# Optimization experiments

Measured on AMD Instinct MI355X. Metric: run time of the kernel, lower is better.

The kernel has to match this reference:

```python
import jax, jax.numpy as jnp
import numpy as np

H = 128; TIME_DIM = 8; LAM = 0.01; NUM_LAYERS = 2; B = 64
N_FACT = 100000; N_COMP = 5000; E = 500000; D_FACT = 384; D_COMP = 64
MLP_IN = 2 + 2 * (TIME_DIM // 2) + 1  # 11


def setup_inputs() -> dict:
    key = jax.random.key(0)
    ks = jax.random.split(key, 40)
    rn = lambda k, sh, s=0.05: jax.random.normal(k, sh, jnp.float32) * s
    inp = {
        'x_fact': jax.random.normal(ks[0], (N_FACT, D_FACT), jnp.float32),
        'x_comp': jax.random.normal(ks[1], (N_COMP, D_COMP), jnp.float32),
        'ea_f2c': jax.random.uniform(ks[2], (E, 2), jnp.float32),
        'ea_c2f': jax.random.uniform(ks[3], (E, 2), jnp.float32),
        'ei_f2c_src': jax.random.randint(ks[4], (E,), 0, N_FACT, jnp.int32),
        'ei_f2c_dst': jax.random.randint(ks[5], (E,), 0, N_COMP, jnp.int32),
        'ei_c2f_src': jax.random.randint(ks[6], (E,), 0, N_COMP, jnp.int32),
        'ei_c2f_dst': jax.random.randint(ks[7], (E,), 0, N_FACT, jnp.int32),
        'fact_batch': jnp.sort(jax.random.randint(ks[8], (N_FACT,), 0, B, jnp.int32)),
        'comp_batch': jnp.sort(jax.random.randint(ks[9], (N_COMP,), 0, B, jnp.int32)),
        # lazy per-type input projections
        'W_in_fact': rn(ks[10], (D_FACT, H)), 'b_in_fact': jnp.zeros((H,), jnp.float32),
        'W_in_comp': rn(ks[11], (D_COMP, H)), 'b_in_comp': jnp.zeros((H,), jnp.float32),
        # EdgeAttrEncoder MLP: 11 -> 32 -> 16 -> 1
        'eW1': rn(ks[12], (MLP_IN, 32)), 'eb1': jnp.zeros((32,), jnp.float32),
        'eW2': rn(ks[13], (32, 16)), 'eb2': jnp.zeros((16,), jnp.float32),
        'eW3': rn(ks[14], (16, 1)), 'eb3': jnp.zeros((1,), jnp.float32),
        # GraphConv per layer (axis0) per edge type (axis1: 0=f->c, 1=c->f)
        'W_rel': rn(ks[15], (NUM_LAYERS, 2, H, H)), 'b_rel': jnp.zeros((NUM_LAYERS, 2, H), jnp.float32),
        'W_root': rn(ks[16], (NUM_LAYERS, 2, H, H)),
        # shared post LayerNorm per node type (axis0: 0=fact, 1=company)
        'ln_scale': jnp.ones((2, H), jnp.float32), 'ln_bias': jnp.zeros((2, H), jnp.float32),
        # classifier 2H -> H -> 1
        'Wc1': rn(ks[17], (2 * H, H)), 'bc1': jnp.zeros((H,), jnp.float32),
        'Wc2': rn(ks[18], (H, 1)), 'bc2': jnp.zeros((1,), jnp.float32),
    }
    return inp


def _edge_gate(ea, eW1, eb1, eW2, eb2, eW3, eb3):
    # ea: [E,2] -> gate [E]
    sent = jnp.clip(ea[:, 0:1], -1.0, 1.0)
    decay = ea[:, 1:2]
    # decay in [0,1] -> delta_t = -log(decay)/lambda, clamped >= 0
    dt = jnp.maximum(-jnp.log(jnp.clip(decay, 1e-6, None)) / LAM, 0.0)
    ds = jnp.clip(dt / 30.0, 0.0, 12.0)
    freqs = jnp.arange(1, TIME_DIM // 2 + 1, dtype=ds.dtype)
    tvec = jnp.concatenate([jnp.sin(ds * freqs), jnp.cos(ds * freqs), ds], axis=-1)
    x = jnp.concatenate([sent, jnp.log1p(dt), tvec], axis=-1)  # [E,11]
    h = jax.nn.relu(x @ eW1 + eb1)
    h = jax.nn.relu(h @ eW2 + eb2)
    return jax.nn.sigmoid(h @ eW3 + eb3)[:, 0]


def _layernorm(x, scale, bias, eps=1e-5):
    mu = jnp.mean(x, axis=-1, keepdims=True)
    var = jnp.var(x, axis=-1, keepdims=True)
    return (x - mu) * jax.lax.rsqrt(var + eps) * scale + bias


def _seg_mean(x, seg, n):
    s = jax.ops.segment_sum(x, seg, num_segments=n)
    c = jax.ops.segment_sum(jnp.ones((x.shape[0], 1), x.dtype), seg, num_segments=n)
    return s / jnp.maximum(c, 1.0)


def reference(x_fact, x_comp, ea_f2c, ea_c2f, ei_f2c_src, ei_f2c_dst, ei_c2f_src,
              ei_c2f_dst, fact_batch, comp_batch, W_in_fact, b_in_fact, W_in_comp,
              b_in_comp, eW1, eb1, eW2, eb2, eW3, eb3, W_rel, b_rel, W_root,
              ln_scale, ln_bias, Wc1, bc1, Wc2, bc2):
    # per-type input projection + ReLU
    xf = jax.nn.relu(x_fact @ W_in_fact + b_in_fact)   # [N_fact, H]
    xc = jax.nn.relu(x_comp @ W_in_comp + b_in_comp)   # [N_comp, H]
    # MLP-gated edge weights (shared encoder across relations)
    w_f2c = _edge_gate(ea_f2c, eW1, eb1, eW2, eb2, eW3, eb3)  # [E]
    w_c2f = _edge_gate(ea_c2f, eW1, eb1, eW2, eb2, eW3, eb3)  # [E]
    nf, nc = xf.shape[0], xc.shape[0]
    for l in range(NUM_LAYERS):
        prev_f, prev_c = xf, xc
        # GraphConv: lin_rel(sum_j w_ij * x_j) + lin_root(x_i)  (aggr='add')
        agg_c = jax.ops.segment_sum(xf[ei_f2c_src] * w_f2c[:, None], ei_f2c_dst, num_segments=nc)
        new_c = agg_c @ W_rel[l, 0] + b_rel[l, 0] + xc @ W_root[l, 0]
        agg_f = jax.ops.segment_sum(xc[ei_c2f_src] * w_c2f[:, None], ei_c2f_dst, num_segments=nf)
        new_f = agg_f @ W_rel[l, 1] + b_rel[l, 1] + xf @ W_root[l, 1]
        # ReLU -> residual -> shared per-type LayerNorm
        xf = _layernorm(jax.nn.relu(new_f) + prev_f, ln_scale[0], ln_bias[0])
        xc = _layernorm(jax.nn.relu(new_c) + prev_c, ln_scale[1], ln_bias[1])
    fact_pool = _seg_mean(xf, fact_batch, B)   # [B, H]
    comp_pool = _seg_mean(xc, comp_batch, B)   # [B, H]
    pooled = jnp.concatenate([fact_pool, comp_pool], axis=-1)  # [B, 2H]
    h = jax.nn.relu(pooled @ Wc1 + bc1)
    return (h @ Wc2 + bc2)[:, 0]  # [B] logits
```

## Files before the change

### kernel.cpp

```cpp
#include <hip/hip_runtime.h>
#include <math.h>

#define H 128
#define EDGES 500000
#define NFACT 100000
#define NCOMP 5000
#define BATCH 64

typedef _Float16 half8_t __attribute__((ext_vector_type(8)));
typedef float floatx4 __attribute__((ext_vector_type(4)));

__device__ inline short4 f4_to_h4(float4 v){
  union { short4 s; _Float16 h[4]; } u;
  u.h[0]=(_Float16)v.x; u.h[1]=(_Float16)v.y; u.h[2]=(_Float16)v.z; u.h[3]=(_Float16)v.w;
  return u.s;
}

__device__ inline half8_t f8_to_h8(float4 a, float4 b){
  half8_t r;
  r[0]=(_Float16)a.x; r[1]=(_Float16)a.y; r[2]=(_Float16)a.z; r[3]=(_Float16)a.w;
  r[4]=(_Float16)b.x; r[5]=(_Float16)b.y; r[6]=(_Float16)b.z; r[7]=(_Float16)b.w;
  return r;
}

__global__ void k_hist(const int* __restrict__ dst, int n, int* __restrict__ cnt){
  for (int e = blockIdx.x*blockDim.x + threadIdx.x; e < n; e += gridDim.x*blockDim.x)
    atomicAdd(&cnt[dst[e]], 1);
}

__global__ __launch_bounds__(1024) void k_scan1(const int* __restrict__ cnt, int n,
                                                int* __restrict__ offs, int* __restrict__ part){
  __shared__ int sh[1024];
  int tid = threadIdx.x;
  int i = blockIdx.x*1024 + tid;
  int v = (i < n) ? cnt[i] : 0;
  sh[tid] = v;
  __syncthreads();
  for (int d = 1; d < 1024; d <<= 1){
    int t = (tid >= d) ? sh[tid-d] : 0;
    __syncthreads();
    sh[tid] += t;
    __syncthreads();
  }
  if (i < n) offs[i] = sh[tid] - v;
  if (tid == 1023) part[blockIdx.x] = sh[1023];
}

__global__ void k_scan2(int* part, int nb){
  __shared__ int sh[128];
  int tid = threadIdx.x;
  int v = (tid < nb) ? part[tid] : 0;
  sh[tid] = v;
  __syncthreads();
  for (int d = 1; d < 128; d <<= 1){
    int t = (tid >= d) ? sh[tid-d] : 0;
    __syncthreads();
    sh[tid] += t;
    __syncthreads();
  }
  if (tid < nb) part[tid] = sh[tid] - v;
}

__global__ __launch_bounds__(1024) void k_scan3(int* offs, int n, const int* __restrict__ part, int total){
  int i = blockIdx.x*1024 + threadIdx.x;
  if (i < n) offs[i] += part[blockIdx.x];
  if (i == 0) offs[n] = total;
}

__global__ void k_fill2(const int* __restrict__ src, const int* __restrict__ dst,
                        const float* __restrict__ w, int n, const int* __restrict__ offs,
                        int* __restrict__ cur, int4* __restrict__ ed){
  for (int e = blockIdx.x*blockDim.x + threadIdx.x; e < n; e += gridDim.x*blockDim.x){
    int d = dst[e];
    int p = offs[d] + atomicAdd(&cur[d], 1);
    ed[p] = make_int4(src[e], __float_as_int(w[e]), d, 0);
  }
}

__global__ __launch_bounds__(256) void k_prep(const float* __restrict__ W_in,
                                              const float* __restrict__ W_rel,
                                              const float* __restrict__ W_root,
                                              _Float16* __restrict__ wt_in,
                                              _Float16* __restrict__ wcat0,
                                              _Float16* __restrict__ wcat1){
  int i = blockIdx.x*256 + threadIdx.x;
  if (i < 49152){
    int n = i / 384, k = i % 384;
    wt_in[i] = (_Float16)W_in[k*128 + n];
  } else if (i < 49152 + 32768){
    int j = i - 49152;
    int n = j / 256, k = j % 256;
    const float* Wr = W_rel  + 1*16384;
    const float* Wo = W_root + 1*16384;
    wcat0[j] = (_Float16)(k < 128 ? Wr[k*128+n] : Wo[(k-128)*128+n]);
  } else if (i < 49152 + 65536){
    int j = i - 49152 - 32768;
    int n = j / 256, k = j % 256;
    const float* Wr = W_rel  + 3*16384;
    const float* Wo = W_root + 3*16384;
    wcat1[j] = (_Float16)(k < 128 ? Wr[k*128+n] : Wo[(k-128)*128+n]);
  }
}

__global__ __launch_bounds__(256) void k_gate(const float* __restrict__ ea,
                       const float* __restrict__ eW1, const float* __restrict__ eb1,
                       const float* __restrict__ eW2, const float* __restrict__ eb2,
                       const float* __restrict__ eW3, const float* __restrict__ eb3,
                       float* __restrict__ wout, int n){
  __shared__ float w1[11*32], b1[32], w2[32*16], b2[16], w3[16];
  __shared__ float b3;
  int tid = threadIdx.x;
  for (int i = tid; i < 11*32; i += blockDim.x) w1[i] = eW1[i];
  for (int i = tid; i < 32;    i += blockDim.x) b1[i] = eb1[i];
  for (int i = tid; i < 32*16; i += blockDim.x) w2[i] = eW2[i];
  for (int i = tid; i < 16;    i += blockDim.x) b2[i] = eb2[i];
  for (int i = tid; i < 16;    i += blockDim.x) w3[i] = eW3[i];
  if (tid == 0) b3 = eb3[0];
  __syncthreads();
  for (int e = blockIdx.x*blockDim.x + tid; e < n; e += gridDim.x*blockDim.x){
    float2 eav = ((const float2*)ea)[e];
    float sent  = fminf(fmaxf(eav.x, -1.f), 1.f);
    float decay = eav.y;
    float dt = fmaxf(-logf(fmaxf(decay, 1e-6f)) * 100.f, 0.f);
    float ds = fminf(dt * (1.f/30.f), 12.f);
    float s1 = sinf(ds), c1 = cosf(ds);
    float s2v = 2.f*s1*c1;
    float c2v = 1.f - 2.f*s1*s1;
    float s3v = s1*c2v + c1*s2v;
    float c3v = c1*c2v - s1*s2v;
    float s4v = 2.f*s2v*c2v;
    float c4v = 1.f - 2.f*s2v*s2v;
    float x[11];
    x[0] = sent; x[1] = log1pf(dt);
    x[2] = s1;  x[3] = s2v; x[4] = s3v; x[5] = s4v;
    x[6] = c1;  x[7] = c2v; x[8] = c3v; x[9] = c4v;
    x[10] = ds;
    float s2[16];
    #pragma unroll
    for (int j = 0; j < 16; j++) s2[j] = b2[j];
    #pragma unroll
    for (int i = 0; i < 32; i++){
      float h = b1[i];
      #pragma unroll
      for (int k = 0; k < 11; k++) h += x[k]*w1[k*32+i];
      h = fmaxf(h, 0.f);
      #pragma unroll
      for (int j = 0; j < 16; j++) s2[j] += h*w2[i*16+j];
    }
    float o = b3;
    #pragma unroll
    for (int j = 0; j < 16; j++) o += fmaxf(s2[j], 0.f)*w3[j];
    wout[e] = 1.f/(1.f + expf(-o));
  }
}

template<int K, int R>
__global__ __launch_bounds__(128) void k_input_s(const float* __restrict__ X, const float* __restrict__ W,
                                                 const float* __restrict__ bias, float* __restrict__ Y){
  __shared__ float xs[R*K];
  int t = threadIdx.x;
  long row0 = (long)blockIdx.x * R;
  const float4* src = (const float4*)(X + row0*K);
  float4* d4 = (float4*)xs;
  for (int i = t; i < R*K/4; i += 128) d4[i] = src[i];
  __syncthreads();
  float acc[R];
  #pragma unroll
  for (int r = 0; r < R; r++) acc[r] = 0.f;
  for (int k4 = 0; k4 < K/4; k4++){
    int kb = k4*4;
    float w0 = W[(kb+0)*H+t], w1 = W[(kb+1)*H+t], w2 = W[(kb+2)*H+t], w3 = W[(kb+3)*H+t];
    #pragma unroll
    for (int r = 0; r < R; r++){
      float4 xv = ((const float4*)(xs + r*K))[k4];
      acc[r] += xv.x*w0 + xv.y*w1 + xv.z*w2 + xv.w*w3;
    }
  }
  float b = bias[t];
  #pragma unroll
  for (int r = 0; r < R; r++)
    Y[(row0+r)*H + t] = fmaxf(acc[r] + b, 0.f);
}

__global__ __launch_bounds__(256, 3) void k_input_m(const float* __restrict__ X,
                                                 const _Float16* __restrict__ Wt,
                                                 const float* __restrict__ bias,
                                                 float* __restrict__ Y){
  int lane = threadIdx.x & 63;
  int wv = threadIdx.x >> 6;
  long row0 = ((long)blockIdx.x*4 + wv) * 16;
  if (row0 >= NFACT) return;
  int m = lane & 15, q = lane >> 4;
  const float4* xrow = (const float4*)(X + (row0 + m)*384 + q*8);
  const _Float16* wb0 = Wt + (size_t)m*384 + q*8;
  float4 xa[12], xb[12];
  #pragma unroll
  for (int ks = 0; ks < 12; ks++){
    xa[ks] = xrow[ks*8];
    xb[ks] = xrow[ks*8 + 1];
  }
  floatx4 acc[8];
  #pragma unroll
  for (int nt = 0; nt < 8; nt++) acc[nt] = (floatx4){0.f,0.f,0.f,0.f};
  #pragma unroll
  for (int ks = 0; ks < 12; ks++){
    half8_t av = f8_to_h8(xa[ks], xb[ks]);
    #pragma unroll
    for (int nt = 0; nt < 8; nt++){
      half8_t bv = *(const half8_t*)(wb0 + (size_t)nt*16*384 + ks*32);
      acc[nt] = __builtin_amdgcn_mfma_f32_16x16x32_f16(av, bv, acc[nt], 0, 0, 0);
    }
  }
  #pragma unroll
  for (int nt = 0; nt < 8; nt++){
    int col = nt*16 + m;
    float b = bias[col];
    #pragma unroll
    for (int i = 0; i < 4; i++)
      Y[(row0 + q*4 + i)*H + col] = fmaxf(acc[nt][i] + b, 0.f);
  }
}

__global__ __launch_bounds__(64) void k_layer_m(
    const float* __restrict__ xsrc, const float* __restrict__ xprev,
    const int* __restrict__ offs, const int4* __restrict__ ed,
    const _Float16* __restrict__ Wt, const float* __restrict__ brel,
    const float* __restrict__ lnsc, const float* __restrict__ lnbi,
    float* __restrict__ xnext){
  __shared__ _Float16 xin[16][264];
  int t = threadIdx.x, c = t & 31, g = t >> 5;
  long row0 = (long)blockIdx.x * 16;
  int grow0 = g*8;
  #pragma unroll
  for (int j = 0; j < 8; j++){
    int lr = grow0 + j;
    ((short4*)&xin[lr][0])[c] = make_short4(0,0,0,0);
    float4 pv = ((const float4*)(xprev + (row0+lr)*H))[c];
    ((short4*)&xin[lr][128])[c] = f4_to_h4(pv);
  }
  int lo = offs[row0 + grow0], hi = offs[row0 + grow0 + 8];
  float4 a = make_float4(0.f,0.f,0.f,0.f);
  int cur = (int)row0 + grow0;
  int idx = lo;
  for (; idx + 8 <= hi; idx += 8){
    int4 mrec[8];
    #pragma unroll
    for (int j = 0; j < 8; j++) mrec[j] = ed[idx+j];
    float4 v[8];
    #pragma unroll
    for (int j = 0; j < 8; j++) v[j] = ((const float4*)(xsrc + (long)mrec[j].x*H))[c];
    #pragma unroll
    for (int j = 0; j < 8; j++){
      float w = __int_as_float(mrec[j].y);
      if (mrec[j].z != cur){ ((short4*)&xin[cur-(int)row0][0])[c] = f4_to_h4(a); a = make_float4(0.f,0.f,0.f,0.f); cur = mrec[j].z; }
      a.x += v[j].x*w; a.y += v[j].y*w; a.z += v[j].z*w; a.w += v[j].w*w;
    }
  }
  for (; idx < hi; idx++){
    int4 mrec = ed[idx];
    float4 v = ((const float4*)(xsrc + (long)mrec.x*H))[c];
    float w = __int_as_float(mrec.y);
    if (mrec.z != cur){ ((short4*)&xin[cur-(int)row0][0])[c] = f4_to_h4(a); a = make_float4(0.f,0.f,0.f,0.f); cur = mrec.z; }
    a.x += v.x*w; a.y += v.y*w; a.z += v.z*w; a.w += v.w*w;
  }
  if (lo < hi) ((short4*)&xin[cur-(int)row0][0])[c] = f4_to_h4(a);

  int m = t & 15, q = t >> 4;
  floatx4 acc[8];
  #pragma unroll
  for (int nt = 0; nt < 8; nt++) acc[nt] = (floatx4){0.f,0.f,0.f,0.f};
  #pragma unroll
  for (int ks = 0; ks < 8; ks++){
    half8_t av = *(const half8_t*)&xin[m][ks*32 + q*8];
    #pragma unroll
    for (int nt = 0; nt < 8; nt++){
      half8_t bv = *(const half8_t*)(Wt + (size_t)(nt*16 + m)*256 + ks*32 + q*8);
      acc[nt] = __builtin_amdgcn_mfma_f32_16x16x32_f16(av, bv, acc[nt], 0, 0, 0);
    }
  }
  float vs[8][4];
  float s[4] = {0.f,0.f,0.f,0.f}, ss[4] = {0.f,0.f,0.f,0.f};
  #pragma unroll
  for (int nt = 0; nt < 8; nt++){
    int col = nt*16 + m;
    float b = brel[col];
    #pragma unroll
    for (int i = 0; i < 4; i++){
      int lr = q*4 + i;
      float pv = (float)xin[lr][128 + col];
      float v = fmaxf(acc[nt][i] + b, 0.f) + pv;
      vs[nt][i] = v;
      s[i] += v; ss[i] += v*v;
    }
  }
  #pragma unroll
  for (int i = 0; i < 4; i++){
    #pragma unroll
    for (int mm = 1; mm < 16; mm <<= 1){
      s[i]  += __shfl_xor(s[i],  mm, 64);
      ss[i] += __shfl_xor(ss[i], mm, 64);
    }
  }
  #pragma unroll
  for (int nt = 0; nt < 8; nt++){
    int col = nt*16 + m;
    float lsc = lnsc[col], lbi = lnbi[col];
    #pragma unroll
    for (int i = 0; i < 4; i++){
      float mu  = s[i]*(1.f/H);
      float var = ss[i]*(1.f/H) - mu*mu;
      float rstd = rsqrtf(var + 1e-5f);
      xnext[(row0 + q*4 + i)*H + col] = (vs[nt][i] - mu)*rstd*lsc + lbi;
    }
  }
}

template<int R>
__global__ __launch_bounds__(128) void k_layer(
    const float* __restrict__ xsrc, const float* __restrict__ xprev,
    const int* __restrict__ offs, const int4* __restrict__ ed,
    const float* __restrict__ Wrel, const float* __restrict__ brel,
    const float* __restrict__ Wroot, const float* __restrict__ lnsc,
    const float* __restrict__ lnbi, float* __restrict__ xnext){
  constexpr int RG = R/4;
  __shared__ float xin[R][256];
  int t = threadIdx.x, c = t & 31, g = t >> 5;
  long row0 = (long)blockIdx.x * R;
  int grow0 = g*RG;
  #pragma unroll
  for (int j = 0; j < RG; j++){
    int lr = grow0 + j;
    ((float4*)&xin[lr][0])[c] = make_float4(0.f,0.f,0.f,0.f);
    ((float4*)&xin[lr][128])[c] = ((const float4*)(xprev + (row0+lr)*H))[c];
  }
  int lo = offs[row0 + grow0], hi = offs[row0 + grow0 + RG];
  float4 a = make_float4(0.f,0.f,0.f,0.f);
  int cur = (int)row0 + grow0;
  int idx = lo;
  for (; idx + 8 <= hi; idx += 8){
    int4 m[8];
    #pragma unroll
    for (int j = 0; j < 8; j++) m[j] = ed[idx+j];
    float4 v[8];
    #pragma unroll
    for (int j = 0; j < 8; j++) v[j] = ((const float4*)(xsrc + (long)m[j].x*H))[c];
    #pragma unroll
    for (int j = 0; j < 8; j++){
      float w = __int_as_float(m[j].y);
      if (m[j].z != cur){ ((float4*)&xin[cur-(int)row0][0])[c] = a; a = make_float4(0.f,0.f,0.f,0.f); cur = m[j].z; }
      a.x += v[j].x*w; a.y += v[j].y*w; a.z += v[j].z*w; a.w += v[j].w*w;
    }
  }
  for (; idx < hi; idx++){
    int4 m = ed[idx];
    float4 v = ((const float4*)(xsrc + (long)m.x*H))[c];
    float w = __int_as_float(m.y);
    if (m.z != cur){ ((float4*)&xin[cur-(int)row0][0])[c] = a; a = make_float4(0.f,0.f,0.f,0.f); cur = m.z; }
    a.x += v.x*w; a.y += v.y*w; a.z += v.z*w; a.w += v.w*w;
  }
  if (lo < hi) ((float4*)&xin[cur-(int)row0][0])[c] = a;

  float4 acc[RG];
  float4 bv = ((const float4*)brel)[c];
  #pragma unroll
  for (int j = 0; j < RG; j++) acc[j] = bv;
  #pragma unroll
  for (int p = 0; p < 2; p++){
    const float4* Wp = (const float4*)(p ? Wroot : Wrel) + c;
    #pragma unroll 4
    for (int k4 = 0; k4 < 32; k4++){
      float4 xv[RG];
      #pragma unroll
      for (int j = 0; j < RG; j++)
        xv[j] = ((const float4*)xin[grow0+j])[p*32 + k4];
      #pragma unroll
      for (int kk = 0; kk < 4; kk++){
        float4 wv = Wp[(size_t)(k4*4+kk)*32];
        #pragma unroll
        for (int j = 0; j < RG; j++){
          float xk = (kk==0) ? xv[j].x : (kk==1) ? xv[j].y : (kk==2) ? xv[j].z : xv[j].w;
          acc[j].x += xk*wv.x; acc[j].y += xk*wv.y; acc[j].z += xk*wv.z; acc[j].w += xk*wv.w;
        }
      }
    }
  }
  float4 lsc = ((const float4*)lnsc)[c];
  float4 lbi = ((const float4*)lnbi)[c];
  #pragma unroll
  for (int j = 0; j < RG; j++){
    int lr = grow0 + j;
    float4 pv = ((const float4*)&xin[lr][128])[c];
    float4 v;
    v.x = fmaxf(acc[j].x, 0.f) + pv.x;
    v.y = fmaxf(acc[j].y, 0.f) + pv.y;
    v.z = fmaxf(acc[j].z, 0.f) + pv.z;
    v.w = fmaxf(acc[j].w, 0.f) + pv.w;
    float s  = v.x + v.y + v.z + v.w;
    float ss = v.x*v.x + v.y*v.y + v.z*v.z + v.w*v.w;
    #pragma unroll
    for (int mm = 1; mm < 32; mm <<= 1){ s += __shfl_xor(s, mm, 64); ss += __shfl_xor(ss, mm, 64); }
    float mu  = s*(1.f/H);
    float var = ss*(1.f/H) - mu*mu;
    float rstd = rsqrtf(var + 1e-5f);
    float4 o;
    o.x = (v.x - mu)*rstd*lsc.x + lbi.x;
    o.y = (v.y - mu)*rstd*lsc.y + lbi.y;
    o.z = (v.z - mu)*rstd*lsc.z + lbi.z;
    o.w = (v.w - mu)*rstd*lsc.w + lbi.w;
    ((float4*)(xnext + (row0+lr)*H))[c] = o;
  }
}

#define PCHUNK 128
#define FBLK ((NFACT + PCHUNK - 1) / PCHUNK)
#define CBLK ((NCOMP + PCHUNK - 1) / PCHUNK)

__global__ __launch_bounds__(128) void k_pool_acc(const float* __restrict__ xf, const float* __restrict__ xc,
                                                  const int* __restrict__ fb, const int* __restrict__ cb,
                                                  float* __restrict__ pooled){
  int t = threadIdx.x;
  int b = blockIdx.x;
  if (b < FBLK){
    int start = b*PCHUNK, end = start + PCHUNK; if (end > NFACT) end = NFACT;
    float s = 0.f; int curb = -1;
    for (int i = start; i < end; i++){
      int bb = fb[i];
      if (bb != curb){
        if (curb >= 0) atomicAdd(&pooled[curb*256 + t], s);
        curb = bb; s = 0.f;
      }
      s += xf[(long)i*H + t];
    }
    if (curb >= 0) atomicAdd(&pooled[curb*256 + t], s);
  } else {
    int bbk = b - FBLK;
    int start = bbk*PCHUNK, end = start + PCHUNK; if (end > NCOMP) end = NCOMP;
    float s = 0.f; int curb = -1;
    for (int i = start; i < end; i++){
      int bb = cb[i];
      if (bb != curb){
        if (curb >= 0) atomicAdd(&pooled[curb*256 + 128 + t], s);
        curb = bb; s = 0.f;
      }
      s += xc[(long)i*H + t];
    }
    if (curb >= 0) atomicAdd(&pooled[curb*256 + 128 + t], s);
  }
}

__device__ inline int lowerb(const int* a, int n, int key){
  int lo = 0, hi = n;
  while (lo < hi){ int m = (lo+hi) >> 1; if (a[m] < key) lo = m+1; else hi = m; }
  return lo;
}

__global__ __launch_bounds__(128) void k_head(const float* __restrict__ pooled,
                                              const int* __restrict__ fb, const int* __restrict__ cb,
                                              const float* __restrict__ Wc1, const float* __restrict__ bc1,
                                              const float* __restrict__ Wc2, const float* __restrict__ bc2,
                                              float* __restrict__ out){
  __shared__ float p[256];
  __shared__ float red[2];
  int t = threadIdx.x, b = blockIdx.x;
  int flo = lowerb(fb, NFACT, b), fhi = lowerb(fb, NFACT, b+1);
  int clo = lowerb(cb, NCOMP, b), chi = lowerb(cb, NCOMP, b+1);
  float fc = (float)((fhi - flo) > 1 ? (fhi - flo) : 1);
  float cc = (float)((chi - clo) > 1 ? (chi - clo) : 1);
  p[t]       = pooled[b*256 + t] / fc;
  p[128 + t] = pooled[b*256 + 128 + t] / cc;
  __syncthreads();
  float acc = bc1[t];
  #pragma unroll 4
  for (int k = 0; k < 256; k++) acc += p[k]*Wc1[k*H + t];
  float h = fmaxf(acc, 0.f)*Wc2[t];
  #pragma unroll
  for (int m = 1; m < 64; m <<= 1) h += __shfl_xor(h, m, 64);
  if ((t & 63) == 0) red[t>>6] = h;
  __syncthreads();
  if (t == 0) out[b] = red[0] + red[1] + bc2[0];
}

extern "C" void kernel_launch(void* const* d_in, const int* in_sizes, int n_in,
                              void* d_out, int out_size, void* d_ws, size_t ws_size,
                              hipStream_t stream){
  const float* x_fact = (const float*)d_in[0];
  const float* x_comp = (const float*)d_in[1];
  const float* ea_f2c = (const float*)d_in[2];
  const float* ea_c2f = (const float*)d_in[3];
  const int* s_f2c   = (const int*)d_in[4];
  const int* dst_f2c = (const int*)d_in[5];
  const int* s_c2f   = (const int*)d_in[6];
  const int* dst_c2f = (const int*)d_in[7];
  const int* fb = (const int*)d_in[8];
  const int* cb = (const int*)d_in[9];
  const float* W_in_f = (const float*)d_in[10];
  const float* b_in_f = (const float*)d_in[11];
  const float* W_in_c = (const float*)d_in[12];
  const float* b_in_c = (const float*)d_in[13];
  const float* eW1 = (const float*)d_in[14]; const float* eb1 = (const float*)d_in[15];
  const float* eW2 = (const float*)d_in[16]; const float* eb2 = (const float*)d_in[17];
  const float* eW3 = (const float*)d_in[18]; const float* eb3 = (const float*)d_in[19];
  const float* W_rel = (const float*)d_in[20]; const float* b_rel = (const float*)d_in[21];
  const float* W_root = (const float*)d_in[22];
  const float* ln_s = (const float*)d_in[23]; const float* ln_b = (const float*)d_in[24];
  const float* Wc1 = (const float*)d_in[25]; const float* bc1 = (const float*)d_in[26];
  const float* Wc2 = (const float*)d_in[27]; const float* bc2 = (const float*)d_in[28];
  float* out = (float*)d_out;

  char* ws = (char*)d_ws;
  size_t off = 0;
  auto alloc = [&](size_t bytes)->char*{ char* p = ws + off; off = (off + bytes + 255) & ~(size_t)255; return p; };
  float* xf0   = (float*)alloc((size_t)NFACT*H*4);
  float* xf1   = (float*)alloc((size_t)NFACT*H*4);
  float* xc0   = (float*)alloc((size_t)NCOMP*H*4);
  float* xc1   = (float*)alloc((size_t)NCOMP*H*4);
  float* w_f2c = (float*)alloc((size_t)EDGES*4);
  float* w_c2f = (float*)alloc((size_t)EDGES*4);
  int4* ed_f2c = (int4*)alloc((size_t)EDGES*16);
  int4* ed_c2f = (int4*)alloc((size_t)EDGES*16);
  int* off_f2c = (int*)alloc((size_t)(NCOMP+1)*4);
  int* cur_f2c = (int*)alloc((size_t)NCOMP*4);
  int* off_c2f = (int*)alloc((size_t)(NFACT+1)*4);
  int* cur_c2f = (int*)alloc((size_t)NFACT*4);
  int* part    = (int*)alloc(128*4);
  float* pooled= (float*)alloc((size_t)BATCH*256*4);
  _Float16* wt_in = (_Float16*)alloc((size_t)49152*2);
  _Float16* wcat0 = (_Float16*)alloc((size_t)32768*2);
  _Float16* wcat1 = (_Float16*)alloc((size_t)32768*2);

  k_prep<<<448,256,0,stream>>>(W_in_f, W_rel, W_root, wt_in, wcat0, wcat1);
  k_gate<<<512,256,0,stream>>>(ea_f2c, eW1,eb1,eW2,eb2,eW3,eb3, w_f2c, EDGES);
  k_gate<<<512,256,0,stream>>>(ea_c2f, eW1,eb1,eW2,eb2,eW3,eb3, w_c2f, EDGES);

  hipMemsetAsync(cur_f2c, 0, NCOMP*4, stream);
  k_hist<<<512,256,0,stream>>>(dst_f2c, EDGES, cur_f2c);
  {
    int nb = (NCOMP + 1023)/1024;
    k_scan1<<<nb,1024,0,stream>>>(cur_f2c, NCOMP, off_f2c, part);
    k_scan2<<<1,128,0,stream>>>(part, nb);
    k_scan3<<<nb,1024,0,stream>>>(off_f2c, NCOMP, part, EDGES);
  }
  hipMemsetAsync(cur_f2c, 0, NCOMP*4, stream);
  k_fill2<<<512,256,0,stream>>>(s_f2c, dst_f2c, w_f2c, EDGES, off_f2c, cur_f2c, ed_f2c);

  hipMemsetAsync(cur_c2f, 0, NFACT*4, stream);
  k_hist<<<512,256,0,stream>>>(dst_c2f, EDGES, cur_c2f);
  {
    int nb = (NFACT + 1023)/1024;
    k_scan1<<<nb,1024,0,stream>>>(cur_c2f, NFACT, off_c2f, part);
    k_scan2<<<1,128,0,stream>>>(part, nb);
    k_scan3<<<nb,1024,0,stream>>>(off_c2f, NFACT, part, EDGES);
  }
  hipMemsetAsync(cur_c2f, 0, NFACT*4, stream);
  k_fill2<<<512,256,0,stream>>>(s_c2f, dst_c2f, w_c2f, EDGES, off_c2f, cur_c2f, ed_c2f);

  k_input_m<<<(NFACT/16 + 3)/4,256,0,stream>>>(x_fact, wt_in, b_in_f, xf0);
  k_input_s<64,8><<<NCOMP/8,128,0,stream>>>(x_comp, W_in_c, b_in_c, xc0);

  const float* xf_p = xf0; const float* xc_p = xc0;
  float* xf_n = xf1; float* xc_n = xc1;
  for (int l = 0; l < 2; l++){
    const float* Wr0 = W_rel  + (size_t)(l*2+0)*H*H;
    const float* br0 = b_rel  + (size_t)(l*2+0)*H;
    const float* br1 = b_rel  + (size_t)(l*2+1)*H;
    const float* Wo0 = W_root + (size_t)(l*2+0)*H*H;
    const _Float16* wcat = (l == 0) ? wcat0 : wcat1;
    k_layer<4><<<NCOMP/4,128,0,stream>>>(xf_p, xc_p, off_f2c, ed_f2c,
                                         Wr0, br0, Wo0, ln_s + H, ln_b + H, xc_n);
    k_layer_m<<<NFACT/16,64,0,stream>>>(xc_p, xf_p, off_c2f, ed_c2f,
                                        wcat, br1, ln_s, ln_b, xf_n);
    const float* tf = xf_p; xf_p = xf_n; xf_n = (float*)tf;
    const float* tc = xc_p; xc_p = xc_n; xc_n = (float*)tc;
  }

  hipMemsetAsync(pooled, 0, (size_t)BATCH*256*4, stream);
  k_pool_acc<<<FBLK + CBLK,128,0,stream>>>(xf_p, xc_p, fb, cb, pooled);
  k_head<<<BATCH,128,0,stream>>>(pooled, fb, cb, Wc1, bc1, Wc2, bc2, out);
}
```

Measured before the change: 966.6 us.

## Make fact input projection persistent with register-resident weights and prefetched LDS tiles

The fact-node input projection kernel becomes persistent over 512 blocks. Each wave keeps its two 16-column slices of the fp16 weight matrix in registers for the whole run, and the block stages 16-row input tiles through shared memory as fp16. The next tile's global load is issued before the MFMA work on the current tile so the load overlaps compute. This removes repeated weight reloads per 16-row tile and improves input load coalescing, at the cost of more registers, lower occupancy (launch bounds 2) and two barriers per tile.

```diff
diff --git a/kernel.cpp b/kernel.cpp
--- a/kernel.cpp
+++ b/kernel.cpp
@@ -6,6 +6,7 @@
 #define NFACT 100000
 #define NCOMP 5000
 #define BATCH 64
+#define NTILE 6250
 
 typedef _Float16 half8_t __attribute__((ext_vector_type(8)));
 typedef float floatx4 __attribute__((ext_vector_type(4)));
@@ -182,42 +183,73 @@
     Y[(row0+r)*H + t] = fmaxf(acc[r] + b, 0.f);
 }
 
-__global__ __launch_bounds__(256, 3) void k_input_m(const float* __restrict__ X,
+__global__ __launch_bounds__(256, 2) void k_input_m(const float* __restrict__ X,
                                                  const _Float16* __restrict__ Wt,
                                                  const float* __restrict__ bias,
                                                  float* __restrict__ Y){
-  int lane = threadIdx.x & 63;
-  int wv = threadIdx.x >> 6;
-  long row0 = ((long)blockIdx.x*4 + wv) * 16;
-  if (row0 >= NFACT) return;
+  __shared__ _Float16 xs[16][392];
+  int t = threadIdx.x;
+  int lane = t & 63, wv = t >> 6;
   int m = lane & 15, q = lane >> 4;
-  const float4* xrow = (const float4*)(X + (row0 + m)*384 + q*8);
-  const _Float16* wb0 = Wt + (size_t)m*384 + q*8;
-  float4 xa[12], xb[12];
-  #pragma unroll
-  for (int ks = 0; ks < 12; ks++){
-    xa[ks] = xrow[ks*8];
-    xb[ks] = xrow[ks*8 + 1];
-  }
-  floatx4 acc[8];
-  #pragma unroll
-  for (int nt = 0; nt < 8; nt++) acc[nt] = (floatx4){0.f,0.f,0.f,0.f};
-  #pragma unroll
-  for (int ks = 0; ks < 12; ks++){
-    half8_t av = f8_to_h8(xa[ks], xb[ks]);
-    #pragma unroll
-    for (int nt = 0; nt < 8; nt++){
-      half8_t bv = *(const half8_t*)(wb0 + (size_t)nt*16*384 + ks*32);
-      acc[nt] = __builtin_amdgcn_mfma_f32_16x16x32_f16(av, bv, acc[nt], 0, 0, 0);
-    }
-  }
-  #pragma unroll
-  for (int nt = 0; nt < 8; nt++){
-    int col = nt*16 + m;
-    float b = bias[col];
-    #pragma unroll
-    for (int i = 0; i < 4; i++)
-      Y[(row0 + q*4 + i)*H + col] = fmaxf(acc[nt][i] + b, 0.f);
+
+  half8_t wreg[2][12];
+  float bcol[2];
+  #pragma unroll
+  for (int j = 0; j < 2; j++){
+    int col = (wv*2 + j)*16 + m;
+    const _Float16* wb = Wt + (size_t)col*384 + q*8;
+    #pragma unroll
+    for (int ks = 0; ks < 12; ks++) wreg[j][ks] = *(const half8_t*)(wb + ks*32);
+    bcol[j] = bias[col];
+  }
+
+  int row_i[6], c4_i[6];
+  #pragma unroll
+  for (int i = 0; i < 6; i++){
+    int idx = i*256 + t;
+    row_i[i] = idx/96; c4_i[i] = idx - row_i[i]*96;
+  }
+
+  int tpb = (NTILE + gridDim.x - 1)/gridDim.x;
+  int tb0 = blockIdx.x*tpb, tb1 = tb0 + tpb;
+  if (tb1 > NTILE) tb1 = NTILE;
+  if (tb0 >= tb1) return;
+
+  const float4* X4 = (const float4*)X;
+  float4 r[6];
+  #pragma unroll
+  for (int i = 0; i < 6; i++) r[i] = X4[(size_t)tb0*1536 + i*256 + t];
+
+  for (int tile = tb0; tile < tb1; ++tile){
+    __syncthreads();
+    #pragma unroll
+    for (int i = 0; i < 6; i++)
+      *(short4*)&xs[row_i[i]][c4_i[i]*4] = f4_to_h4(r[i]);
+    __syncthreads();
+    if (tile + 1 < tb1){
+      size_t base = (size_t)(tile+1)*1536;
+      #pragma unroll
+      for (int i = 0; i < 6; i++) r[i] = X4[base + i*256 + t];
+    }
+    __builtin_amdgcn_sched_barrier(0);
+
+    floatx4 acc0 = (floatx4){0.f,0.f,0.f,0.f};
+    floatx4 acc1 = (floatx4){0.f,0.f,0.f,0.f};
+    #pragma unroll
+    for (int ks = 0; ks < 12; ks++){
+      half8_t av = *(const half8_t*)&xs[m][ks*32 + q*8];
+      acc0 = __builtin_amdgcn_mfma_f32_16x16x32_f16(av, wreg[0][ks], acc0, 0, 0, 0);
+      acc1 = __builtin_amdgcn_mfma_f32_16x16x32_f16(av, wreg[1][ks], acc1, 0, 0, 0);
+    }
+    long rb = (long)tile*16;
+    #pragma unroll
+    for (int j = 0; j < 2; j++){
+      floatx4 a = j ? acc1 : acc0;
+      int col = (wv*2 + j)*16 + m;
+      #pragma unroll
+      for (int i2 = 0; i2 < 4; i2++)
+        Y[(rb + q*4 + i2)*H + col] = fmaxf(a[i2] + bcol[j], 0.f);
+    }
   }
 }
 
@@ -554,7 +586,7 @@
   hipMemsetAsync(cur_c2f, 0, NFACT*4, stream);
   k_fill2<<<512,256,0,stream>>>(s_c2f, dst_c2f, w_c2f, EDGES, off_c2f, cur_c2f, ed_c2f);
 
-  k_input_m<<<(NFACT/16 + 3)/4,256,0,stream>>>(x_fact, wt_in, b_in_f, xf0);
+  k_input_m<<<512,256,0,stream>>>(x_fact, wt_in, b_in_f, xf0);
   k_input_s<64,8><<<NCOMP/8,128,0,stream>>>(x_comp, W_in_c, b_in_c, xc0);
 
   const float* xf_p = xf0; const float* xc_p = xc0;
```

New measurement: 919.9 us. 1.05x faster.
